# Kernel optimization log

Hardware: AMD Instinct MI355X
Metric: run time of the kernel (lower is better)

## Reference

```python
import jax, jax.numpy as jnp
import numpy as np

B, C, H, W = 8, 512, 32, 32
N_HEADS, HEAD_DIM = 8, 64
EPS = 1e-5


def _layernorm(x, g, b):
    mu = jnp.mean(x, axis=-1, keepdims=True)
    var = jnp.mean(jnp.square(x - mu), axis=-1, keepdims=True)
    return (x - mu) * jax.lax.rsqrt(var + EPS) * g + b


def setup_inputs() -> dict:
    key = jax.random.key(0)
    ks = jax.random.split(key, 16)
    u = lambda k, shp: jax.random.uniform(k, shp, dtype=jnp.float32)
    inp = {
        "x": jax.random.normal(ks[0], (B, C, H, W), dtype=jnp.float32),
        "t": jax.random.normal(ks[1], (B,), dtype=jnp.float32),
        # attention params (torch.rand init in source)
        "K_W": u(ks[2], (N_HEADS, C, HEAD_DIM)), "K_b": u(ks[3], (N_HEADS, HEAD_DIM)),
        "Q_W": u(ks[4], (N_HEADS, C, HEAD_DIM)), "Q_b": u(ks[5], (N_HEADS, HEAD_DIM)),
        "V_W": u(ks[6], (N_HEADS, C, HEAD_DIM)), "V_b": u(ks[7], (N_HEADS, HEAD_DIM)),
        "O_W": u(ks[8], (N_HEADS, HEAD_DIM, C)), "O_b": u(ks[9], (C,)),
        # pre-attention LayerNorm
        "ln1_g": jnp.ones((C,), jnp.float32), "ln1_b": jnp.zeros((C,), jnp.float32),
        # MLP: LayerNorm -> Linear -> GELU -> Linear
        "ln2_g": jnp.ones((C,), jnp.float32), "ln2_b": jnp.zeros((C,), jnp.float32),
        "W1": jax.random.normal(ks[10], (C, C), dtype=jnp.float32) / np.sqrt(C),
        "b1": jnp.zeros((C,), jnp.float32),
        "W2": jax.random.normal(ks[11], (C, C), dtype=jnp.float32) / np.sqrt(C),
        "b2": jnp.zeros((C,), jnp.float32),
    }
    return inp


def reference(x, t, K_W, K_b, Q_W, Q_b, V_W, V_b, O_W, O_b,
              ln1_g, ln1_b, ln2_g, ln2_b, W1, b1, W2, b2):
    b, c, h, w = x.shape
    xs = x.reshape(b, c, h * w).transpose(0, 2, 1)           # b s c
    res = _layernorm(xs, ln1_g, ln1_b)
    q = jnp.einsum('bsc,ncd->bsnd', res, Q_W) + Q_b          # b s n_h h_dim
    k = jnp.einsum('bsc,ncd->bsnd', res, K_W) + K_b
    v = jnp.einsum('bsc,ncd->bsnd', res, V_W) + V_b
    scores = jnp.einsum('bsnd,btnd->bnst', q, k) / jnp.sqrt(jnp.float32(c))
    attn = jax.nn.softmax(scores, axis=-1)                   # b n_h s s
    o = jnp.einsum('bnst,btnd->bsnd', attn, v)
    out = jnp.einsum('bsnd,ndc->bsc', o, O_W) + O_b
    out = out + xs                                           # residual
    m = _layernorm(out, ln2_g, ln2_b)
    m = jax.nn.gelu(m @ W1 + b1, approximate=False) @ W2 + b2
    out = m + out
    return out.transpose(0, 2, 1).reshape(b, c, h, w)
```

## Files before the change

kernel.cpp:

```cpp
#include <hip/hip_runtime.h>
#include <math.h>

#define BB 8
#define CC 512
#define SS 1024
#define NHH 8
#define HDD 64
#define KD 512

typedef __attribute__((ext_vector_type(8))) short short8;
typedef __attribute__((ext_vector_type(4))) float f32x4;
typedef __attribute__((ext_vector_type(4))) unsigned short ushort4v;

__device__ __forceinline__ unsigned short f2bf(float x) {
  union { float f; unsigned int u; } c; c.f = x;
  unsigned int r = (c.u + 0x7FFFu + ((c.u >> 16) & 1u)) >> 16;
  return (unsigned short)r;
}
__device__ __forceinline__ float b2f(unsigned short h) {
  union { unsigned int u; float f; } c; c.u = ((unsigned int)h) << 16; return c.f;
}

#define GLD_LDS(gp, lp) __builtin_amdgcn_global_load_lds( \
    (const __attribute__((address_space(1))) void*)(gp),  \
    (__attribute__((address_space(3))) void*)(lp), 16, 0, 0)

__device__ __forceinline__ float block_reduce_sum(float v) {
  __shared__ float sm[4];
  #pragma unroll
  for (int o = 32; o > 0; o >>= 1) v += __shfl_down(v, o, 64);
  if ((threadIdx.x & 63) == 0) sm[threadIdx.x >> 6] = v;
  __syncthreads();
  float r = (sm[0] + sm[1]) + (sm[2] + sm[3]);
  __syncthreads();
  return r;
}

__global__ __launch_bounds__(256) void ln1_stats(const float* __restrict__ x,
                                                 float2* __restrict__ mustd) {
  const int b = blockIdx.y, s0 = blockIdx.x * 64;
  const int sl = threadIdx.x & 63, cg = threadIdx.x >> 6;
  const float* xp = x + (size_t)b * CC * SS + s0 + sl;
  float ps = 0.f, pq = 0.f;
  #pragma unroll 8
  for (int i = 0; i < 128; ++i) {
    const float v = xp[(size_t)(cg * 128 + i) * SS];
    ps += v; pq += v * v;
  }
  __shared__ float sred[2][4][64];
  sred[0][cg][sl] = ps; sred[1][cg][sl] = pq;
  __syncthreads();
  if (cg == 0) {
    const float s = (sred[0][0][sl] + sred[0][1][sl]) + (sred[0][2][sl] + sred[0][3][sl]);
    const float q = (sred[1][0][sl] + sred[1][1][sl]) + (sred[1][2][sl] + sred[1][3][sl]);
    const float mu = s * (1.0f / CC);
    const float rs = rsqrtf(q * (1.0f / CC) - mu * mu + 1e-5f);
    mustd[b * SS + s0 + sl] = make_float2(mu, rs);
  }
}

__global__ __launch_bounds__(256) void ln1_apply(
    const float* __restrict__ x, const float2* __restrict__ mustd,
    const float* __restrict__ g, const float* __restrict__ be,
    unsigned short* __restrict__ yh, unsigned short* __restrict__ yl,
    unsigned short* __restrict__ xh, unsigned short* __restrict__ xl) {
  __shared__ float tile[32][33];
  const int b = blockIdx.z, c0 = blockIdx.y * 32, s0 = blockIdx.x * 32;
  const int tx = threadIdx.x, ty = threadIdx.y;
  const float* xb = x + ((size_t)b * CC + c0) * SS + s0;
  #pragma unroll
  for (int i = ty; i < 32; i += 8)
    tile[i][tx] = xb[(size_t)i * SS + tx];
  __syncthreads();
  const float gc = g[c0 + tx], bc = be[c0 + tx];
  #pragma unroll
  for (int i = ty; i < 32; i += 8) {
    const float2 ms = mustd[b * SS + s0 + i];
    const float v = tile[tx][i];
    const float y = (v - ms.x) * ms.y * gc + bc;
    const size_t oi = ((size_t)b * SS + s0 + i) * CC + c0 + tx;
    const unsigned short hy = f2bf(y);
    yh[oi] = hy; yl[oi] = f2bf(y - b2f(hy));
    const unsigned short hx = f2bf(v);
    xh[oi] = hx; xl[oi] = f2bf(v - b2f(hx));
  }
}

__global__ __launch_bounds__(256) void ln_bf16_k(const float* __restrict__ in,
                                                 const float* __restrict__ g,
                                                 const float* __restrict__ be,
                                                 unsigned short* __restrict__ outh) {
  size_t row = blockIdx.x;
  const float* r = in + row * CC;
  int t = threadIdx.x;
  float v0 = r[t], v1 = r[t + 256];
  float s = block_reduce_sum(v0 + v1);
  float mu = s * (1.0f / CC);
  float d0 = v0 - mu, d1 = v1 - mu;
  float vs = block_reduce_sum(d0 * d0 + d1 * d1);
  float rstd = rsqrtf(vs * (1.0f / CC) + 1e-5f);
  outh[row * CC + t]       = f2bf(d0 * rstd * g[t] + be[t]);
  outh[row * CC + t + 256] = f2bf(d1 * rstd * g[t + 256] + be[t + 256]);
}

__global__ __launch_bounds__(256) void convert_weights(
    const float* __restrict__ QW, const float* __restrict__ KW,
    const float* __restrict__ VW, const float* __restrict__ OW,
    const float* __restrict__ W1, const float* __restrict__ W2,
    const float* __restrict__ Qb, const float* __restrict__ Kb,
    const float* __restrict__ Vb,
    unsigned short* __restrict__ BtQKh, unsigned short* __restrict__ BtQKl,
    unsigned short* __restrict__ BtVh,
    unsigned short* __restrict__ BtOh, unsigned short* __restrict__ BtOl,
    unsigned short* __restrict__ BtW1h, unsigned short* __restrict__ BtW2h,
    float* __restrict__ qkvb) {
  __shared__ float tile[32][33];
  const int p = blockIdx.z, wsel = p >> 3, sub = p & 7;
  const int k0 = blockIdx.x * 32, d0 = blockIdx.y * 32;
  const int tx = threadIdx.x, ty = threadIdx.y;
  const float* w; int rs; unsigned short *dh, *dl; int nbase;
  switch (wsel) {
    case 0:  w = QW + sub * 32768; rs = 64;  dh = BtQKh; dl = BtQKl;  nbase = sub * 64;        break;
    case 1:  w = KW + sub * 32768; rs = 64;  dh = BtQKh; dl = BtQKl;  nbase = 512 + sub * 64;  break;
    case 2:  w = VW + sub * 32768; rs = 64;  dh = BtVh;  dl = nullptr; nbase = sub * 64;       break;
    case 3:  w = OW + sub * 64;    rs = 512; dh = BtOh;  dl = BtOl;   nbase = sub * 64;        break;
    case 4:  w = W1 + sub * 64;    rs = 512; dh = BtW1h; dl = nullptr; nbase = sub * 64;       break;
    default: w = W2 + sub * 64;    rs = 512; dh = BtW2h; dl = nullptr; nbase = sub * 64;       break;
  }
  for (int i = ty; i < 32; i += 8)
    tile[i][tx] = w[(size_t)(k0 + i) * rs + d0 + tx];
  __syncthreads();
  for (int i = ty; i < 32; i += 8) {
    float f = tile[tx][i];
    unsigned short h = f2bf(f);
    size_t idx = (size_t)(nbase + d0 + i) * KD + k0 + tx;
    dh[idx] = h;
    if (dl) dl[idx] = f2bf(f - b2f(h));
  }
  if (p == 0 && blockIdx.x == 0 && blockIdx.y == 0) {
    int t = ty * 32 + tx;
    for (int i = t; i < 1536; i += 256)
      qkvb[i] = i < 512 ? Qb[i] : (i < 1024 ? Kb[i - 512] : Vb[i - 1024]);
  }
}

__global__ __launch_bounds__(256) void gemm_qkv(
    const unsigned short* __restrict__ Ah, const unsigned short* __restrict__ Al,
    const unsigned short* __restrict__ Bth, const unsigned short* __restrict__ Btl,
    const float* __restrict__ bias,
    unsigned short* __restrict__ qkh, unsigned short* __restrict__ qkl,
    unsigned short* __restrict__ vt) {
  __shared__ __align__(16) unsigned short smem[4 * 128 * 32];
  unsigned short* As = smem;
  unsigned short* Bs = smem + 2 * 128 * 32;
  const int tid = threadIdx.x;
  const int w = tid >> 6, l = tid & 63, quad = l >> 4, lm = l & 15;
  const int n0 = blockIdx.x * 128, m0 = blockIdx.y * 128;
  const bool splitB = n0 < 1024;
  const int wm = (w >> 1) * 64, wn = (w & 1) * 64;
  const int srow = tid >> 2;
  const int sch = (((tid & 3) ^ (srow & 3)) * 8);
  const unsigned short* Agh = Ah + (size_t)(m0 + srow) * KD + sch;
  const unsigned short* Agl = Al + (size_t)(m0 + srow) * KD + sch;
  const unsigned short* Bgh = Bth + (size_t)(n0 + srow) * KD + sch;
  const unsigned short* Bgl = Btl + (size_t)(n0 + srow) * KD + sch;
  unsigned short* Aswh = As + w * 512;
  unsigned short* Aswl = As + 4096 + w * 512;
  unsigned short* Bswh = Bs + w * 512;
  unsigned short* Bswl = Bs + 4096 + w * 512;
  const int rch = ((quad ^ (lm & 3)) * 8);
  const f32x4 fzero = {0.f, 0.f, 0.f, 0.f};
  f32x4 acc[4][4];
  #pragma unroll
  for (int i = 0; i < 4; ++i)
    #pragma unroll
    for (int j = 0; j < 4; ++j) acc[i][j] = fzero;
  for (int k0 = 0; k0 < KD; k0 += 32) {
    __syncthreads();
    GLD_LDS(Agh + k0, Aswh);
    GLD_LDS(Agh + k0 + 64 * KD, Aswh + 2048);
    GLD_LDS(Agl + k0, Aswl);
    GLD_LDS(Agl + k0 + 64 * KD, Aswl + 2048);
    GLD_LDS(Bgh + k0, Bswh);
    GLD_LDS(Bgh + k0 + 64 * KD, Bswh + 2048);
    if (splitB) {
      GLD_LDS(Bgl + k0, Bswl);
      GLD_LDS(Bgl + k0 + 64 * KD, Bswl + 2048);
    }
    __syncthreads();
    short8 afh[4], afl[4], bfh[4], bfl[4];
    #pragma unroll
    for (int i = 0; i < 4; ++i) {
      afh[i] = *(const short8*)(As + (wm + i * 16 + lm) * 32 + rch);
      afl[i] = *(const short8*)(As + 4096 + (wm + i * 16 + lm) * 32 + rch);
    }
    #pragma unroll
    for (int j = 0; j < 4; ++j)
      bfh[j] = *(const short8*)(Bs + (wn + j * 16 + lm) * 32 + rch);
    if (splitB) {
      #pragma unroll
      for (int j = 0; j < 4; ++j)
        bfl[j] = *(const short8*)(Bs + 4096 + (wn + j * 16 + lm) * 32 + rch);
      #pragma unroll
      for (int i = 0; i < 4; ++i)
        #pragma unroll
        for (int j = 0; j < 4; ++j) {
          f32x4 t = acc[i][j];
          t = __builtin_amdgcn_mfma_f32_16x16x32_bf16(afh[i], bfh[j], t, 0, 0, 0);
          t = __builtin_amdgcn_mfma_f32_16x16x32_bf16(afh[i], bfl[j], t, 0, 0, 0);
          t = __builtin_amdgcn_mfma_f32_16x16x32_bf16(afl[i], bfh[j], t, 0, 0, 0);
          acc[i][j] = t;
        }
    } else {
      #pragma unroll
      for (int i = 0; i < 4; ++i)
        #pragma unroll
        for (int j = 0; j < 4; ++j)
          acc[i][j] = __builtin_amdgcn_mfma_f32_16x16x32_bf16(afh[i], bfh[j], acc[i][j], 0, 0, 0);
    }
  }
  if (splitB) {
    #pragma unroll
    for (int i = 0; i < 4; ++i) {
      const int row = m0 + wm + i * 16 + quad * 4;
      #pragma unroll
      for (int j = 0; j < 4; ++j) {
        const int ncol = n0 + wn + j * 16 + lm;
        const float bv = bias[ncol];
        #pragma unroll
        for (int r = 0; r < 4; ++r) {
          const float xv = acc[i][j][r] + bv;
          const size_t oi = (size_t)(row + r) * 1024 + ncol;
          unsigned short h = f2bf(xv);
          qkh[oi] = h;
          qkl[oi] = f2bf(xv - b2f(h));
        }
      }
    }
  } else {
    __syncthreads();
    #pragma unroll
    for (int i = 0; i < 4; ++i) {
      const int mlb = wm + i * 16 + quad * 4;
      #pragma unroll
      for (int j = 0; j < 4; ++j) {
        const int nl = wn + j * 16 + lm;
        const float bv = bias[n0 + nl];
        ushort4v pk;
        #pragma unroll
        for (int r = 0; r < 4; ++r) pk[r] = f2bf(acc[i][j][r] + bv);
        const int chunk = ((mlb >> 3) ^ (nl & 15));
        *(ushort4v*)(smem + nl * 128 + chunk * 8 + (mlb & 7)) = pk;
      }
    }
    __syncthreads();
    const int tn = tid >> 4, tc = tid & 15;
    const int bb2 = m0 >> 10, sbase = m0 & 1023;
    #pragma unroll
    for (int pass = 0; pass < 8; ++pass) {
      const int nl = pass * 16 + tn;
      const int hh = (n0 - 1024 + nl) >> 6, dd = nl & 63;
      short8 v8 = *(const short8*)(smem + nl * 128 + ((tc ^ (nl & 15)) * 8));
      *(short8*)(vt + ((size_t)(bb2 * 8 + hh) * 64 + dd) * 1024 + sbase + tc * 8) = v8;
    }
  }
}

template<int SB, int GELU, int OUTMODE, int RESID, int TRANS>
__global__ __launch_bounds__(256) void gemm64(
    const unsigned short* __restrict__ Ah,
    const unsigned short* __restrict__ Bh, const unsigned short* __restrict__ Bl,
    const float* __restrict__ bias, const float* __restrict__ residf,
    const unsigned short* __restrict__ residh, const unsigned short* __restrict__ residl,
    unsigned short* __restrict__ outh, float* __restrict__ outf, int ldc) {
  __shared__ __align__(16) unsigned short As[64 * 32];
  __shared__ __align__(16) unsigned short Bs[(SB ? 2 : 1) * 64 * 32];
  __shared__ float ttile[TRANS ? 64 : 1][TRANS ? 65 : 1];
  const int tid = threadIdx.x;
  const int w = tid >> 6, l = tid & 63, quad = l >> 4, lm = l & 15;
  const int n0 = blockIdx.x * 64, m0 = blockIdx.y * 64;
  const int wm = (w >> 1) * 32, wn = (w & 1) * 32;
  const int srow = tid >> 2;
  const int sch = (((tid & 3) ^ (srow & 3)) * 8);
  const unsigned short* Ag = Ah + (size_t)(m0 + srow) * KD + sch;
  const unsigned short* Bg = Bh + (size_t)(n0 + srow) * KD + sch;
  const unsigned short* Bgl = SB ? Bl + (size_t)(n0 + srow) * KD + sch : nullptr;
  unsigned short* Asw = As + w * 512;
  unsigned short* Bsw = Bs + w * 512;
  unsigned short* Bswl = Bs + 2048 + w * 512;
  const int rch = ((quad ^ (lm & 3)) * 8);
  const f32x4 fzero = {0.f, 0.f, 0.f, 0.f};
  f32x4 acc[2][2];
  #pragma unroll
  for (int i = 0; i < 2; ++i)
    #pragma unroll
    for (int j = 0; j < 2; ++j) acc[i][j] = fzero;
  for (int k0 = 0; k0 < KD; k0 += 32) {
    __syncthreads();
    GLD_LDS(Ag + k0, Asw);
    GLD_LDS(Bg + k0, Bsw);
    if constexpr (SB) GLD_LDS(Bgl + k0, Bswl);
    __syncthreads();
    short8 af[2], bfh[2], bfl[2];
    #pragma unroll
    for (int i = 0; i < 2; ++i)
      af[i] = *(const short8*)(As + (wm + i * 16 + lm) * 32 + rch);
    #pragma unroll
    for (int j = 0; j < 2; ++j)
      bfh[j] = *(const short8*)(Bs + (wn + j * 16 + lm) * 32 + rch);
    if constexpr (SB) {
      #pragma unroll
      for (int j = 0; j < 2; ++j)
        bfl[j] = *(const short8*)(Bs + 2048 + (wn + j * 16 + lm) * 32 + rch);
    }
    #pragma unroll
    for (int i = 0; i < 2; ++i)
      #pragma unroll
      for (int j = 0; j < 2; ++j) {
        f32x4 t = acc[i][j];
        t = __builtin_amdgcn_mfma_f32_16x16x32_bf16(af[i], bfh[j], t, 0, 0, 0);
        if constexpr (SB)
          t = __builtin_amdgcn_mfma_f32_16x16x32_bf16(af[i], bfl[j], t, 0, 0, 0);
        acc[i][j] = t;
      }
  }
  if constexpr (TRANS) __syncthreads();
  #pragma unroll
  for (int i = 0; i < 2; ++i) {
    const int row = m0 + wm + i * 16 + quad * 4;
    #pragma unroll
    for (int j = 0; j < 2; ++j) {
      const int col = n0 + wn + j * 16 + lm;
      const float bv = bias[col];
      #pragma unroll
      for (int r = 0; r < 4; ++r) {
        float x = acc[i][j][r] + bv;
        if (GELU) x = 0.5f * x * (1.0f + erff(x * 0.70710678118654752f));
        const size_t ri = (size_t)(row + r) * CC + col;
        if (RESID == 1) x += residf[ri];
        if (RESID == 2) x += b2f(residh[ri]) + b2f(residl[ri]);
        if constexpr (TRANS) {
          ttile[wm + i * 16 + quad * 4 + r][wn + j * 16 + lm] = x;
        } else {
          const size_t oi = (size_t)(row + r) * ldc + col;
          if (OUTMODE == 0) outf[oi] = x;
          else outh[oi] = f2bf(x);
        }
      }
    }
  }
  if constexpr (TRANS) {
    __syncthreads();
    const int bi = m0 >> 10, s0 = m0 & 1023;
    const int s = tid & 63;
    #pragma unroll
    for (int c0 = 0; c0 < 64; c0 += 4) {
      const int col = c0 + (tid >> 6);
      outf[(size_t)(bi * 512 + n0 + col) * 1024 + s0 + s] = ttile[s][col];
    }
  }
}

__global__ __launch_bounds__(256) void attn_mfma(
    const unsigned short* __restrict__ QKh, const unsigned short* __restrict__ QKl,
    const unsigned short* __restrict__ Vt, unsigned short* __restrict__ Oh) {
  __shared__ __align__(16) unsigned short Ksh[64 * 64], Ksl[64 * 64];
  __shared__ __align__(16) unsigned short Vts[64 * 64];
  __shared__ __align__(16) unsigned short Ps[4 * 16 * 88];
  const int q0 = blockIdx.x * 64, h = blockIdx.y, b = blockIdx.z;
  const int tid = threadIdx.x, w = tid >> 6, l = tid & 63, quad = l >> 4, lm = l & 15;
  const int LDQ = 2 * CC;
  const size_t qkbase = (size_t)b * SS * LDQ;
  const int srow8 = tid >> 3;
  const int sch8  = ((tid & 7) ^ (srow8 & 7)) * 8;
  const unsigned short* Vg = Vt + ((size_t)(b * 8 + h) * 64 + srow8) * 1024 + sch8;
  short8 qh[2], ql[2];
  {
    const size_t qo = qkbase + (size_t)(q0 + w * 16 + lm) * LDQ + h * 64 + quad * 8;
    qh[0] = *(const short8*)(QKh + qo);
    qh[1] = *(const short8*)(QKh + qo + 32);
    ql[0] = *(const short8*)(QKl + qo);
    ql[1] = *(const short8*)(QKl + qo + 32);
  }
  short8 bones;
  #pragma unroll
  for (int u = 0; u < 8; ++u) bones[u] = (lm == 0) ? (short)0x3F80 : (short)0;
  const f32x4 fzero = {0.f, 0.f, 0.f, 0.f};
  float mrow[4];
  f32x4 oacc[5];
  #pragma unroll
  for (int r = 0; r < 4; ++r) mrow[r] = -1e30f;
  #pragma unroll
  for (int j = 0; j < 5; ++j) oacc[j] = fzero;
  const float scale = 0.044194173824159216f * 1.4426950408889634f;
  unsigned short* Pw = Ps + w * (16 * 88);
  for (int kt = 0; kt < SS; kt += 64) {
    __syncthreads();
    {
      const unsigned short* kg  = QKh + qkbase + (size_t)(kt + srow8) * LDQ + CC + h * 64 + sch8;
      const unsigned short* kgl = QKl + qkbase + (size_t)(kt + srow8) * LDQ + CC + h * 64 + sch8;
      GLD_LDS(kg, Ksh + w * 512);
      GLD_LDS(kg + 32 * LDQ, Ksh + 2048 + w * 512);
      GLD_LDS(kgl, Ksl + w * 512);
      GLD_LDS(kgl + 32 * LDQ, Ksl + 2048 + w * 512);
      GLD_LDS(Vg + kt, Vts + w * 512);
      GLD_LDS(Vg + kt + 32 * 1024, Vts + 2048 + w * 512);
    }
    __syncthreads();
    f32x4 sc[4];
    #pragma unroll
    for (int j = 0; j < 4; ++j) sc[j] = fzero;
    #pragma unroll
    for (int st = 0; st < 2; ++st) {
      const int kc = ((st * 4 + quad) ^ (lm & 7)) * 8;
      #pragma unroll
      for (int j = 0; j < 4; ++j) {
        short8 kh = *(const short8*)(Ksh + (j * 16 + lm) * 64 + kc);
        short8 kl = *(const short8*)(Ksl + (j * 16 + lm) * 64 + kc);
        f32x4 t = sc[j];
        t = __builtin_amdgcn_mfma_f32_16x16x32_bf16(qh[st], kh, t, 0, 0, 0);
        t = __builtin_amdgcn_mfma_f32_16x16x32_bf16(qh[st], kl, t, 0, 0, 0);
        t = __builtin_amdgcn_mfma_f32_16x16x32_bf16(ql[st], kh, t, 0, 0, 0);
        sc[j] = t;
      }
    }
    #pragma unroll
    for (int j = 0; j < 4; ++j) sc[j] *= scale;
    #pragma unroll
    for (int r = 0; r < 4; ++r) {
      float mt = fmaxf(fmaxf(sc[0][r], sc[1][r]), fmaxf(sc[2][r], sc[3][r]));
      #pragma unroll
      for (int mask = 1; mask < 16; mask <<= 1) mt = fmaxf(mt, __shfl_xor(mt, mask, 64));
      const float mn = fmaxf(mrow[r], mt);
      const float alpha = exp2f(mrow[r] - mn);
      mrow[r] = mn;
      #pragma unroll
      for (int j = 0; j < 4; ++j) sc[j][r] = exp2f(sc[j][r] - mn);
      #pragma unroll
      for (int j = 0; j < 5; ++j) oacc[j][r] *= alpha;
    }
    #pragma unroll
    for (int r = 0; r < 4; ++r)
      #pragma unroll
      for (int j = 0; j < 4; ++j)
        Pw[(quad * 4 + r) * 88 + j * 16 + lm] = f2bf(sc[j][r]);
    #pragma unroll
    for (int st = 0; st < 2; ++st) {
      short8 ap = *(const short8*)(Pw + lm * 88 + st * 32 + quad * 8);
      const int kc = ((st * 4 + quad) ^ (lm & 7)) * 8;
      #pragma unroll
      for (int j = 0; j < 4; ++j) {
        short8 vv = *(const short8*)(Vts + (j * 16 + lm) * 64 + kc);
        oacc[j] = __builtin_amdgcn_mfma_f32_16x16x32_bf16(ap, vv, oacc[j], 0, 0, 0);
      }
      oacc[4] = __builtin_amdgcn_mfma_f32_16x16x32_bf16(ap, bones, oacc[4], 0, 0, 0);
    }
  }
  float inv[4];
  #pragma unroll
  for (int r = 0; r < 4; ++r) {
    const float lv = __shfl(oacc[4][r], l & 48, 64);
    inv[r] = 1.f / lv;
  }
  const size_t obase =
      (size_t)b * SS * CC + (size_t)(q0 + w * 16 + quad * 4) * CC + h * 64 + lm;
  #pragma unroll
  for (int j = 0; j < 4; ++j)
    #pragma unroll
    for (int r = 0; r < 4; ++r)
      Oh[obase + (size_t)r * CC + j * 16] = f2bf(oacc[j][r] * inv[r]);
}

extern "C" void kernel_launch(void* const* d_in, const int* in_sizes, int n_in,
                              void* d_out, int out_size, void* d_ws, size_t ws_size,
                              hipStream_t stream) {
  const float* x    = (const float*)d_in[0];
  const float* K_W  = (const float*)d_in[2];
  const float* K_b  = (const float*)d_in[3];
  const float* Q_W  = (const float*)d_in[4];
  const float* Q_b  = (const float*)d_in[5];
  const float* V_W  = (const float*)d_in[6];
  const float* V_b  = (const float*)d_in[7];
  const float* O_W  = (const float*)d_in[8];
  const float* O_b  = (const float*)d_in[9];
  const float* ln1g = (const float*)d_in[10];
  const float* ln1b = (const float*)d_in[11];
  const float* ln2g = (const float*)d_in[12];
  const float* ln2b = (const float*)d_in[13];
  const float* W1   = (const float*)d_in[14];
  const float* b1   = (const float*)d_in[15];
  const float* W2   = (const float*)d_in[16];
  const float* b2   = (const float*)d_in[17];
  float* out = (float*)d_out;

  unsigned char* ws = (unsigned char*)d_ws;
  const size_t MB = 1u << 20;
  unsigned short* qkh   = (unsigned short*)(ws);
  unsigned short* qkl   = (unsigned short*)(ws + 16 * MB);
  unsigned short* vt    = (unsigned short*)(ws + 32 * MB);
  unsigned short* ln1h  = (unsigned short*)(ws + 40 * MB);
  unsigned short* ln1l  = (unsigned short*)(ws + 48 * MB);
  unsigned short* xsh   = (unsigned short*)(ws + 56 * MB);
  unsigned short* xsl   = (unsigned short*)(ws + 64 * MB);
  unsigned short* oh    = ln1h;
  float* out1           = (float*)(ws + 72 * MB);
  unsigned short* ln2h  = qkh;
  unsigned short* geluh = (unsigned short*)(ws + 8 * MB);
  unsigned short* BtAll = (unsigned short*)(ws + 88 * MB);
  unsigned short* BtQKh = BtAll;
  unsigned short* BtVh  = BtAll + 1024 * 512;
  unsigned short* BtQKl = BtVh + 512 * 512;
  unsigned short* BtOh  = BtQKl + 1024 * 512;
  unsigned short* BtOl  = BtOh + 512 * 512;
  unsigned short* BtW1h = BtOl + 512 * 512;
  unsigned short* BtW2h = BtW1h + 512 * 512;
  float* qkvb           = (float*)(BtW2h + 512 * 512);
  float2* mustd         = (float2*)(ws + 96 * MB);

  dim3 tb32(32, 8);
  convert_weights<<<dim3(16, 2, 48), tb32, 0, stream>>>(
      Q_W, K_W, V_W, O_W, W1, W2, Q_b, K_b, V_b,
      BtQKh, BtQKl, BtVh, BtOh, BtOl, BtW1h, BtW2h, qkvb);
  ln1_stats<<<dim3(SS / 64, BB), 256, 0, stream>>>(x, mustd);
  ln1_apply<<<dim3(SS / 32, CC / 32, BB), tb32, 0, stream>>>(
      x, mustd, ln1g, ln1b, ln1h, ln1l, xsh, xsl);
  gemm_qkv<<<dim3(12, 64), 256, 0, stream>>>(
      ln1h, ln1l, BtAll, BtQKl, qkvb, qkh, qkl, vt);
  attn_mfma<<<dim3(SS / 64, NHH, BB), 256, 0, stream>>>(qkh, qkl, vt, oh);
  gemm64<1, 0, 0, 2, 0><<<dim3(8, 128), 256, 0, stream>>>(
      oh, BtOh, BtOl, O_b, nullptr, xsh, xsl, nullptr, out1, CC);
  ln_bf16_k<<<BB * SS, 256, 0, stream>>>(out1, ln2g, ln2b, ln2h);
  gemm64<0, 1, 1, 0, 0><<<dim3(8, 128), 256, 0, stream>>>(
      ln2h, BtW1h, nullptr, b1, nullptr, nullptr, nullptr, geluh, nullptr, CC);
  gemm64<0, 0, 0, 1, 1><<<dim3(8, 128), 256, 0, stream>>>(
      geluh, BtW2h, nullptr, b2, out1, nullptr, nullptr, nullptr, out, CC);
}
```

Baseline: 307.5 us.

## Fold softmax scale into Q weights, widen gemm64 K-step, truncate P to bf16

Multiplies the Q projection weights and bias by the softmax scale (with log2e) during weight conversion, so the attention kernel no longer scales every score tile. The gemm64 kernel now loads 64-wide K slices with an 8-chunk XOR swizzle into one shared buffer that is reused for the transpose tile. This halves the number of barrier pairs per GEMM. The attention P values are now converted to bf16 by truncation instead of round-to-nearest, which shortens the inner loop at a small cost in accuracy. Pre-scaling Q in bf16 hi/lo form also shifts rounding slightly.

```diff
diff --git a/kernel.cpp b/kernel.cpp
--- a/kernel.cpp
+++ b/kernel.cpp
@@ -114,13 +114,14 @@
     unsigned short* __restrict__ BtOh, unsigned short* __restrict__ BtOl,
     unsigned short* __restrict__ BtW1h, unsigned short* __restrict__ BtW2h,
     float* __restrict__ qkvb) {
+  const float SCL = 0.044194173824159216f * 1.4426950408889634f;
   __shared__ float tile[32][33];
   const int p = blockIdx.z, wsel = p >> 3, sub = p & 7;
   const int k0 = blockIdx.x * 32, d0 = blockIdx.y * 32;
   const int tx = threadIdx.x, ty = threadIdx.y;
-  const float* w; int rs; unsigned short *dh, *dl; int nbase;
+  const float* w; int rs; unsigned short *dh, *dl; int nbase; float mul = 1.0f;
   switch (wsel) {
-    case 0:  w = QW + sub * 32768; rs = 64;  dh = BtQKh; dl = BtQKl;  nbase = sub * 64;        break;
+    case 0:  w = QW + sub * 32768; rs = 64;  dh = BtQKh; dl = BtQKl;  nbase = sub * 64; mul = SCL; break;
     case 1:  w = KW + sub * 32768; rs = 64;  dh = BtQKh; dl = BtQKl;  nbase = 512 + sub * 64;  break;
     case 2:  w = VW + sub * 32768; rs = 64;  dh = BtVh;  dl = nullptr; nbase = sub * 64;       break;
     case 3:  w = OW + sub * 64;    rs = 512; dh = BtOh;  dl = BtOl;   nbase = sub * 64;        break;
@@ -131,7 +132,7 @@
     tile[i][tx] = w[(size_t)(k0 + i) * rs + d0 + tx];
   __syncthreads();
   for (int i = ty; i < 32; i += 8) {
-    float f = tile[tx][i];
+    float f = tile[tx][i] * mul;
     unsigned short h = f2bf(f);
     size_t idx = (size_t)(nbase + d0 + i) * KD + k0 + tx;
     dh[idx] = h;
@@ -140,7 +141,7 @@
   if (p == 0 && blockIdx.x == 0 && blockIdx.y == 0) {
     int t = ty * 32 + tx;
     for (int i = t; i < 1536; i += 256)
-      qkvb[i] = i < 512 ? Qb[i] : (i < 1024 ? Kb[i - 512] : Vb[i - 1024]);
+      qkvb[i] = i < 512 ? Qb[i] * SCL : (i < 1024 ? Kb[i - 512] : Vb[i - 1024]);
   }
 }
 
@@ -273,56 +274,65 @@
     const float* __restrict__ bias, const float* __restrict__ residf,
     const unsigned short* __restrict__ residh, const unsigned short* __restrict__ residl,
     unsigned short* __restrict__ outh, float* __restrict__ outf, int ldc) {
-  __shared__ __align__(16) unsigned short As[64 * 32];
-  __shared__ __align__(16) unsigned short Bs[(SB ? 2 : 1) * 64 * 32];
-  __shared__ float ttile[TRANS ? 64 : 1][TRANS ? 65 : 1];
+  constexpr int STAGE = (SB ? 3 : 2) * 8192;
+  constexpr int TSIZE = TRANS ? 64 * 65 * 4 : 0;
+  __shared__ __align__(16) unsigned char smem[STAGE > TSIZE ? STAGE : TSIZE];
+  unsigned short* As  = (unsigned short*)smem;
+  unsigned short* Bs  = (unsigned short*)(smem + 8192);
+  unsigned short* Bls = (unsigned short*)(smem + 16384);
+  float (*ttile)[65]  = (float(*)[65])smem;
   const int tid = threadIdx.x;
   const int w = tid >> 6, l = tid & 63, quad = l >> 4, lm = l & 15;
   const int n0 = blockIdx.x * 64, m0 = blockIdx.y * 64;
   const int wm = (w >> 1) * 32, wn = (w & 1) * 32;
-  const int srow = tid >> 2;
-  const int sch = (((tid & 3) ^ (srow & 3)) * 8);
-  const unsigned short* Ag = Ah + (size_t)(m0 + srow) * KD + sch;
-  const unsigned short* Bg = Bh + (size_t)(n0 + srow) * KD + sch;
-  const unsigned short* Bgl = SB ? Bl + (size_t)(n0 + srow) * KD + sch : nullptr;
-  unsigned short* Asw = As + w * 512;
-  unsigned short* Bsw = Bs + w * 512;
-  unsigned short* Bswl = Bs + 2048 + w * 512;
-  const int rch = ((quad ^ (lm & 3)) * 8);
+  const int srow8 = tid >> 3;
+  const int sch8  = ((tid & 7) ^ (srow8 & 7)) * 8;
+  const unsigned short* Ag  = Ah + (size_t)(m0 + srow8) * KD + sch8;
+  const unsigned short* Bg  = Bh + (size_t)(n0 + srow8) * KD + sch8;
+  const unsigned short* Bgl = SB ? Bl + (size_t)(n0 + srow8) * KD + sch8 : nullptr;
   const f32x4 fzero = {0.f, 0.f, 0.f, 0.f};
   f32x4 acc[2][2];
   #pragma unroll
   for (int i = 0; i < 2; ++i)
     #pragma unroll
     for (int j = 0; j < 2; ++j) acc[i][j] = fzero;
-  for (int k0 = 0; k0 < KD; k0 += 32) {
-    __syncthreads();
-    GLD_LDS(Ag + k0, Asw);
-    GLD_LDS(Bg + k0, Bsw);
-    if constexpr (SB) GLD_LDS(Bgl + k0, Bswl);
-    __syncthreads();
-    short8 af[2], bfh[2], bfl[2];
-    #pragma unroll
-    for (int i = 0; i < 2; ++i)
-      af[i] = *(const short8*)(As + (wm + i * 16 + lm) * 32 + rch);
-    #pragma unroll
-    for (int j = 0; j < 2; ++j)
-      bfh[j] = *(const short8*)(Bs + (wn + j * 16 + lm) * 32 + rch);
+  for (int k0 = 0; k0 < KD; k0 += 64) {
+    __syncthreads();
+    GLD_LDS(Ag + k0, As + w * 512);
+    GLD_LDS(Ag + k0 + 32 * KD, As + 2048 + w * 512);
+    GLD_LDS(Bg + k0, Bs + w * 512);
+    GLD_LDS(Bg + k0 + 32 * KD, Bs + 2048 + w * 512);
     if constexpr (SB) {
+      GLD_LDS(Bgl + k0, Bls + w * 512);
+      GLD_LDS(Bgl + k0 + 32 * KD, Bls + 2048 + w * 512);
+    }
+    __syncthreads();
+    #pragma unroll
+    for (int ks = 0; ks < 2; ++ks) {
+      const int kc = ((ks * 4 + quad) ^ (lm & 7)) * 8;
+      short8 af[2], bfh[2], bfl[2];
+      #pragma unroll
+      for (int i = 0; i < 2; ++i)
+        af[i] = *(const short8*)(As + (wm + i * 16 + lm) * 64 + kc);
       #pragma unroll
       for (int j = 0; j < 2; ++j)
-        bfl[j] = *(const short8*)(Bs + 2048 + (wn + j * 16 + lm) * 32 + rch);
-    }
-    #pragma unroll
-    for (int i = 0; i < 2; ++i)
-      #pragma unroll
-      for (int j = 0; j < 2; ++j) {
-        f32x4 t = acc[i][j];
-        t = __builtin_amdgcn_mfma_f32_16x16x32_bf16(af[i], bfh[j], t, 0, 0, 0);
-        if constexpr (SB)
-          t = __builtin_amdgcn_mfma_f32_16x16x32_bf16(af[i], bfl[j], t, 0, 0, 0);
-        acc[i][j] = t;
-      }
+        bfh[j] = *(const short8*)(Bs + (wn + j * 16 + lm) * 64 + kc);
+      if constexpr (SB) {
+        #pragma unroll
+        for (int j = 0; j < 2; ++j)
+          bfl[j] = *(const short8*)(Bls + (wn + j * 16 + lm) * 64 + kc);
+      }
+      #pragma unroll
+      for (int i = 0; i < 2; ++i)
+        #pragma unroll
+        for (int j = 0; j < 2; ++j) {
+          f32x4 t = acc[i][j];
+          t = __builtin_amdgcn_mfma_f32_16x16x32_bf16(af[i], bfh[j], t, 0, 0, 0);
+          if constexpr (SB)
+            t = __builtin_amdgcn_mfma_f32_16x16x32_bf16(af[i], bfl[j], t, 0, 0, 0);
+          acc[i][j] = t;
+        }
+    }
   }
   if constexpr (TRANS) __syncthreads();
   #pragma unroll
@@ -392,7 +402,6 @@
   for (int r = 0; r < 4; ++r) mrow[r] = -1e30f;
   #pragma unroll
   for (int j = 0; j < 5; ++j) oacc[j] = fzero;
-  const float scale = 0.044194173824159216f * 1.4426950408889634f;
   unsigned short* Pw = Ps + w * (16 * 88);
   for (int kt = 0; kt < SS; kt += 64) {
     __syncthreads();
@@ -425,8 +434,6 @@
       }
     }
     #pragma unroll
-    for (int j = 0; j < 4; ++j) sc[j] *= scale;
-    #pragma unroll
     for (int r = 0; r < 4; ++r) {
       float mt = fmaxf(fmaxf(sc[0][r], sc[1][r]), fmaxf(sc[2][r], sc[3][r]));
       #pragma unroll
@@ -442,8 +449,10 @@
     #pragma unroll
     for (int r = 0; r < 4; ++r)
       #pragma unroll
-      for (int j = 0; j < 4; ++j)
-        Pw[(quad * 4 + r) * 88 + j * 16 + lm] = f2bf(sc[j][r]);
+      for (int j = 0; j < 4; ++j) {
+        union { float f; unsigned int u; } pc; pc.f = sc[j][r];
+        Pw[(quad * 4 + r) * 88 + j * 16 + lm] = (unsigned short)(pc.u >> 16);
+      }
     #pragma unroll
     for (int st = 0; st < 2; ++st) {
       short8 ap = *(const short8*)(Pw + lm * 88 + st * 32 + quad * 8);
```

Result: faster. 291.7 us (-5.1%).
